# Kernel optimization log

Hardware: AMD Instinct MI355X
Metric: run time of the kernel (lower is better)

## Reference

```python
import jax, jax.numpy as jnp
import numpy as np

N = 8192
E = 262144
IN_F = 256
OUT_F = 64
H = 2
SLOPE = 0.2
NEG = -9e15


def _xavier(key, shape, gain):
    fan_in, fan_out = shape[-2], shape[-1]
    a = gain * np.sqrt(6.0 / (fan_in + fan_out))
    return jax.random.uniform(key, shape, jnp.float32, -a, a)


def setup_inputs() -> dict:
    key = jax.random.key(0)
    k_x, k_e, k_w, k_a1, k_a2 = jax.random.split(key, 5)
    gain = np.sqrt(2.0)
    return {
        "x": jax.random.normal(k_x, (N, IN_F), jnp.float32),
        "edge_index": jax.random.randint(k_e, (2, E), 0, N, jnp.int64),
        # per-head params (torch Linear stores weight [out,in]; we store [in,out])
        "W": _xavier(k_w, (H, IN_F, OUT_F), gain),
        "a1": _xavier(k_a1, (H, OUT_F), gain),
        "a2": _xavier(k_a2, (H, OUT_F), gain),
    }


def reference(x, edge_index, W, a1, a2):
    n = x.shape[0]
    # dense adjacency mask from COO edges (to_dense_adj: adj[src, dst] += 1; only adj>0 matters)
    adj = jnp.zeros((n, n), jnp.float32).at[edge_index[0], edge_index[1]].add(1.0)
    mask = adj > 0  # [N, N]

    xh = jnp.einsum('ni,hio->hno', x, W)          # [H, N, out]
    s1 = jnp.einsum('hno,ho->hn', xh, a1)          # a1(x): [H, N]
    s2 = jnp.einsum('hno,ho->hn', xh, a2)          # a2(x): [H, N]
    e = jnp.where(mask[None], s1[:, :, None] + s2[:, None, :], NEG)  # [H, N, N]
    e = jnp.where(e >= 0, e, SLOPE * e)            # leaky_relu
    att = jax.nn.softmax(e, axis=-1)               # [H, N, N]
    out = jnp.einsum('hnm,hmo->hno', att, xh)      # [H, N, out]
    # concat heads along feature dim (is_final_layer=False)
    return jnp.transpose(out, (1, 0, 2)).reshape(n, H * OUT_F)
```

## Files before the change

kernel.cpp:

```cpp
#include <hip/hip_runtime.h>

#define NN    8192
#define INF_  256
#define OUTF  64
#define NH    2
#define NE    262144
#define CAP   256
#define SLOPE 0.2f

typedef __attribute__((ext_vector_type(8))) short short8;
typedef __attribute__((ext_vector_type(4))) float f32x4;
typedef __attribute__((ext_vector_type(2))) long long ll2;

__device__ __forceinline__ unsigned short f2bf(float f) {
  unsigned int u = __float_as_uint(f);
  u += 0x7fffu + ((u >> 16) & 1u);
  return (unsigned short)(u >> 16);
}

__global__ __launch_bounds__(256) void prep_kernel(const float* __restrict__ W,
                                                   const unsigned int* __restrict__ ei,
                                                   unsigned short* __restrict__ Bt,
                                                   int* __restrict__ deg,
                                                   int* __restrict__ flag) {
  const int b = blockIdx.x, t = threadIdx.x;
  if (b < 128) {
    const int c = b, k = t;
    Bt[c * 256 + k] = f2bf(W[(c >> 6) * (INF_ * OUTF) + k * OUTF + (c & 63)]);
  } else if (b < 160) {
    deg[(b - 128) * 256 + t] = 0;
  } else {
    __shared__ int nz;
    if (t == 0) nz = 0;
    __syncthreads();
    if (ei[2u * t + 1u] != 0u) atomicAdd(&nz, 1);
    __syncthreads();
    if (t == 0) *flag = (nz == 0) ? 1 : 0;
  }
}

__global__ __launch_bounds__(256) void xh_mfma_kernel(const float* __restrict__ x,
                                                      const unsigned short* __restrict__ Bt,
                                                      const float* __restrict__ a1,
                                                      const float* __restrict__ a2,
                                                      float* __restrict__ xh,
                                                      float* __restrict__ s1,
                                                      float* __restrict__ s2) {
  const int t = threadIdx.x;
  const int l = t & 63, w = t >> 6;
  const int lo = l & 15, hi = l >> 4;
  const int n0 = blockIdx.x * 16;
  const int tcb = w * 2;
  __shared__ float p1s[4][16], p2s[4][16];

  const float* xp = x + (size_t)(n0 + lo) * INF_ + hi * 8;
  float4 fr[16];
#pragma unroll
  for (int ks = 0; ks < 8; ++ks) {
    fr[2 * ks]     = *(const float4*)(xp + ks * 32);
    fr[2 * ks + 1] = *(const float4*)(xp + ks * 32 + 4);
  }
  short8 afr[8];
#pragma unroll
  for (int ks = 0; ks < 8; ++ks) {
    short8 a;
    a[0] = (short)f2bf(fr[2 * ks].x);     a[1] = (short)f2bf(fr[2 * ks].y);
    a[2] = (short)f2bf(fr[2 * ks].z);     a[3] = (short)f2bf(fr[2 * ks].w);
    a[4] = (short)f2bf(fr[2 * ks + 1].x); a[5] = (short)f2bf(fr[2 * ks + 1].y);
    a[6] = (short)f2bf(fr[2 * ks + 1].z); a[7] = (short)f2bf(fr[2 * ks + 1].w);
    afr[ks] = a;
  }
  f32x4 acc[2] = {};
#pragma unroll
  for (int ks = 0; ks < 8; ++ks) {
#pragma unroll
    for (int q = 0; q < 2; ++q) {
      const short8 bf = *(const short8*)(Bt + (size_t)((tcb + q) * 16 + lo) * INF_ + ks * 32 + hi * 8);
      acc[q] = __builtin_amdgcn_mfma_f32_16x16x32_bf16(afr[ks], bf, acc[q], 0, 0, 0);
    }
  }
  float a1c[2], a2c[2];
#pragma unroll
  for (int q = 0; q < 2; ++q) {
    const int tc = tcb + q;
    const int h = tc >> 2;
    const int col = (tc * 16 + lo) & 63;
    a1c[q] = a1[h * OUTF + col];
    a2c[q] = a2[h * OUTF + col];
#pragma unroll
    for (int r = 0; r < 4; ++r)
      xh[((size_t)h * NN + n0 + hi * 4 + r) * OUTF + col] = acc[q][r];
  }
#pragma unroll
  for (int r = 0; r < 4; ++r) {
    float p1 = acc[0][r] * a1c[0] + acc[1][r] * a1c[1];
    float p2 = acc[0][r] * a2c[0] + acc[1][r] * a2c[1];
#pragma unroll
    for (int s = 1; s < 16; s <<= 1) {
      p1 += __shfl_xor(p1, s, 64);
      p2 += __shfl_xor(p2, s, 64);
    }
    if (lo == 0) {
      p1s[w][hi * 4 + r] = p1;
      p2s[w][hi * 4 + r] = p2;
    }
  }
  __syncthreads();
  if (t < 16) {
    s1[n0 + t]      = p1s[0][t] + p1s[1][t];
    s1[NN + n0 + t] = p1s[2][t] + p1s[3][t];
    s2[n0 + t]      = p2s[0][t] + p2s[1][t];
    s2[NN + n0 + t] = p2s[2][t] + p2s[3][t];
  }
}

__global__ __launch_bounds__(256) void edge_kernel(const int* __restrict__ ei,
                                                   const int* __restrict__ flag,
                                                   int* __restrict__ deg,
                                                   int* __restrict__ cols) {
  const int e0 = (blockIdx.x * 256 + threadIdx.x) * 2;
  if (e0 >= NE) return;
  int i0, j0, i1, j1;
  if (*flag) {
    const ll2 a = *(const ll2*)((const long long*)ei + e0);
    const ll2 b = *(const ll2*)((const long long*)ei + NE + e0);
    i0 = (int)a[0]; i1 = (int)a[1]; j0 = (int)b[0]; j1 = (int)b[1];
  } else {
    const int2 a = *(const int2*)(ei + e0);
    const int2 b = *(const int2*)(ei + NE + e0);
    i0 = a.x; i1 = a.y; j0 = b.x; j1 = b.y;
  }
  const int p0 = atomicAdd(&deg[i0], 1);
  if (p0 < CAP) cols[i0 * CAP + p0] = j0;
  const int p1 = atomicAdd(&deg[i1], 1);
  if (p1 < CAP) cols[i1 * CAP + p1] = j1;
}

__global__ __launch_bounds__(128) void agg_kernel(const float* __restrict__ xh,
                                                  const float* __restrict__ s1,
                                                  const float* __restrict__ s2,
                                                  const int* __restrict__ deg,
                                                  const int* __restrict__ cols,
                                                  float* __restrict__ out) {
  const int i = blockIdx.x;
  const int t = threadIdx.x;
  const int h = t >> 6, lane = t & 63;
  __shared__ unsigned int bm[NN / 32];
  __shared__ unsigned long long vmask;
  __shared__ int   cjs[CAP];
  __shared__ float wts[NH][CAP];
  int d = deg[i];
  if (d > CAP) d = CAP;
  bm[t] = 0u; bm[t + 128] = 0u;
  __syncthreads();

  const float* base = xh + (size_t)h * NN * OUTF;
  const int c4 = lane & 15, r = lane >> 4;

  if (d == 0) {
    f32x4 acc = {0.f, 0.f, 0.f, 0.f};
    for (int p = r; p < NN; p += 4)
      acc += *(const f32x4*)(base + (size_t)p * OUTF + 4 * c4);
#pragma unroll
    for (int c = 0; c < 4; ++c) {
      acc[c] += __shfl_xor(acc[c], 16, 64);
      acc[c] += __shfl_xor(acc[c], 32, 64);
    }
    if (lane < 16) {
      const float sc = 1.f / (float)NN;
      float4 o;
      o.x = acc[0] * sc; o.y = acc[1] * sc; o.z = acc[2] * sc; o.w = acc[3] * sc;
      *(float4*)(out + (size_t)i * (NH * OUTF) + h * OUTF + 4 * lane) = o;
    }
    return;
  }

  if (d <= 64) {
    int j = 0;
    const bool valid = lane < d;
    if (valid) j = cols[i * CAP + lane];
    if (h == 0) {
      bool dup = false;
      if (valid) {
        const unsigned int old = atomicOr(&bm[j >> 5], 1u << (j & 31));
        dup = (old >> (j & 31)) & 1u;
      }
      const unsigned long long bal = __ballot(valid && !dup);
      if (lane == 0) vmask = bal;
    }
    __syncthreads();
    const bool kp = (vmask >> lane) & 1ull;
    float sc = -1e30f;
    if (kp) {
      sc = s1[h * NN + i] + s2[h * NN + j];
      sc = (sc >= 0.f) ? sc : SLOPE * sc;
    }
    float m = sc;
#pragma unroll
    for (int s = 32; s > 0; s >>= 1) m = fmaxf(m, __shfl_xor(m, s, 64));
    const float wt = kp ? __expf(sc - m) : 0.f;
    float ds = wt;
#pragma unroll
    for (int s = 32; s > 0; s >>= 1) ds += __shfl_xor(ds, s, 64);
    const float inv = 1.f / ds;

    f32x4 acc = {0.f, 0.f, 0.f, 0.f};
#pragma unroll 2
    for (int p = 0; p < d; p += 4) {
      const int pr = p + r;
      float ww = __shfl(wt, pr, 64);
      int   jj = __shfl(j,  pr, 64);
      ww = (pr < d) ? ww : 0.f;
      jj = (ww > 0.f) ? jj : 0;
      const f32x4 v = *(const f32x4*)(base + (size_t)jj * OUTF + 4 * c4);
      acc += ww * v;
    }
#pragma unroll
    for (int c = 0; c < 4; ++c) {
      acc[c] += __shfl_xor(acc[c], 16, 64);
      acc[c] += __shfl_xor(acc[c], 32, 64);
    }
    if (lane < 16) {
      float4 o;
      o.x = acc[0] * inv; o.y = acc[1] * inv; o.z = acc[2] * inv; o.w = acc[3] * inv;
      *(float4*)(out + (size_t)i * (NH * OUTF) + h * OUTF + 4 * lane) = o;
    }
    return;
  }

  for (int p = t; p < d; p += 128) cjs[p] = cols[i * CAP + p];
  __syncthreads();
  if (h == 0) {
    for (int p = lane; p < d; p += 64) {
      const int j = cjs[p];
      const unsigned int old = atomicOr(&bm[j >> 5], 1u << (j & 31));
      if ((old >> (j & 31)) & 1u) cjs[p] = -1;
    }
  }
  __syncthreads();
  const float s1i = s1[h * NN + i];
  float m = -1e30f;
  for (int p = lane; p < d; p += 64) {
    const int j = cjs[p];
    float sc = -1e30f;
    if (j >= 0) {
      sc = s1i + s2[h * NN + j];
      sc = (sc >= 0.f) ? sc : SLOPE * sc;
    }
    wts[h][p] = sc;
    m = fmaxf(m, sc);
  }
#pragma unroll
  for (int s = 32; s > 0; s >>= 1) m = fmaxf(m, __shfl_xor(m, s, 64));
  float ds = 0.f;
  for (int p = lane; p < d; p += 64) {
    const float sc = wts[h][p];
    const float w2 = (sc > -1e29f) ? __expf(sc - m) : 0.f;
    wts[h][p] = w2;
    ds += w2;
  }
#pragma unroll
  for (int s = 32; s > 0; s >>= 1) ds += __shfl_xor(ds, s, 64);
  const float inv = 1.f / ds;
  float acc = 0.f;
  for (int p = 0; p < d; ++p) {
    const float w2 = wts[h][p];
    if (w2 > 0.f) acc += w2 * base[(size_t)cjs[p] * OUTF + lane];
  }
  out[(size_t)i * (NH * OUTF) + h * OUTF + lane] = acc * inv;
}

extern "C" void kernel_launch(void* const* d_in, const int* in_sizes, int n_in,
                              void* d_out, int out_size, void* d_ws, size_t ws_size,
                              hipStream_t stream) {
  const float* x  = (const float*)d_in[0];
  const int*   ei = (const int*)d_in[1];
  const float* W  = (const float*)d_in[2];
  const float* a1 = (const float*)d_in[3];
  const float* a2 = (const float*)d_in[4];
  float* out = (float*)d_out;

  char* ws = (char*)d_ws;
  float*          xh  = (float*)(ws);
  float*          s1  = (float*)(ws + (4u << 20));
  float*          s2  = (float*)(ws + (4u << 20) + (64u << 10));
  int*            deg = (int*)  (ws + (4u << 20) + (128u << 10));
  int*            cols= (int*)  (ws + (4u << 20) + (192u << 10));
  unsigned short* Bt  = (unsigned short*)(ws + (12u << 20) + (192u << 10));
  int*            flag= (int*)  (ws + (12u << 20) + (256u << 10));

  prep_kernel<<<161, 256, 0, stream>>>(W, (const unsigned int*)ei, Bt, deg, flag);
  xh_mfma_kernel<<<NN / 16, 256, 0, stream>>>(x, Bt, a1, a2, xh, s1, s2);
  edge_kernel<<<NE / 512, 256, 0, stream>>>(ei, flag, deg, cols);
  agg_kernel<<<NN, 128, 0, stream>>>(xh, s1, s2, deg, cols, out);
}
```

Measured before the change: 52.47 us.

## Map one wavefront per node-head task and pad degree counters to cut atomic contention

The aggregation kernel changes from one 128-thread block per node to a grid-stride loop that gives each wavefront one (node, head) task. Duplicate detection moves from an LDS bitmap with atomics and block syncs to a shuffle-based pairwise compare, and the large-degree path now recomputes scores instead of staging them in shared memory. Degree counters are padded to a 16-int stride so atomics on different nodes land on separate cache lines, and s1/s2 are stored interleaved per head as float2. The aim is to remove block-level syncs, the LDS bitmap clear, and atomic contention, at the cost of quadratic dedup work on high-degree nodes.

```diff
diff --git a/kernel.cpp b/kernel.cpp
--- a/kernel.cpp
+++ b/kernel.cpp
@@ -6,6 +6,7 @@
 #define NH    2
 #define NE    262144
 #define CAP   256
+#define DEGS  16
 #define SLOPE 0.2f
 
 typedef __attribute__((ext_vector_type(8))) short short8;
@@ -28,7 +29,9 @@
     const int c = b, k = t;
     Bt[c * 256 + k] = f2bf(W[(c >> 6) * (INF_ * OUTF) + k * OUTF + (c & 63)]);
   } else if (b < 160) {
-    deg[(b - 128) * 256 + t] = 0;
+    int4* dp = (int4*)(deg + (size_t)(b - 128) * 4096 + t * 16);
+    const int4 z = {0, 0, 0, 0};
+    dp[0] = z; dp[1] = z; dp[2] = z; dp[3] = z;
   } else {
     __shared__ int nz;
     if (t == 0) nz = 0;
@@ -44,8 +47,8 @@
                                                       const float* __restrict__ a1,
                                                       const float* __restrict__ a2,
                                                       float* __restrict__ xh,
-                                                      float* __restrict__ s1,
-                                                      float* __restrict__ s2) {
+                                                      float2* __restrict__ s1v,
+                                                      float2* __restrict__ s2v) {
   const int t = threadIdx.x;
   const int l = t & 63, w = t >> 6;
   const int lo = l & 15, hi = l >> 4;
@@ -107,10 +110,11 @@
   }
   __syncthreads();
   if (t < 16) {
-    s1[n0 + t]      = p1s[0][t] + p1s[1][t];
-    s1[NN + n0 + t] = p1s[2][t] + p1s[3][t];
-    s2[n0 + t]      = p2s[0][t] + p2s[1][t];
-    s2[NN + n0 + t] = p2s[2][t] + p2s[3][t];
+    float2 v1, v2;
+    v1.x = p1s[0][t] + p1s[1][t];  v1.y = p1s[2][t] + p1s[3][t];
+    v2.x = p2s[0][t] + p2s[1][t];  v2.y = p2s[2][t] + p2s[3][t];
+    s1v[n0 + t] = v1;
+    s2v[n0 + t] = v2;
   }
 }
 
@@ -130,90 +134,117 @@
     const int2 b = *(const int2*)(ei + NE + e0);
     i0 = a.x; i1 = a.y; j0 = b.x; j1 = b.y;
   }
-  const int p0 = atomicAdd(&deg[i0], 1);
+  const int p0 = atomicAdd(&deg[i0 * DEGS], 1);
   if (p0 < CAP) cols[i0 * CAP + p0] = j0;
-  const int p1 = atomicAdd(&deg[i1], 1);
+  const int p1 = atomicAdd(&deg[i1 * DEGS], 1);
   if (p1 < CAP) cols[i1 * CAP + p1] = j1;
 }
 
-__global__ __launch_bounds__(128) void agg_kernel(const float* __restrict__ xh,
-                                                  const float* __restrict__ s1,
-                                                  const float* __restrict__ s2,
+__global__ __launch_bounds__(256) void agg_kernel(const float* __restrict__ xh,
+                                                  const float2* __restrict__ s1v,
+                                                  const float2* __restrict__ s2v,
                                                   const int* __restrict__ deg,
                                                   const int* __restrict__ cols,
                                                   float* __restrict__ out) {
-  const int i = blockIdx.x;
   const int t = threadIdx.x;
-  const int h = t >> 6, lane = t & 63;
-  __shared__ unsigned int bm[NN / 32];
-  __shared__ unsigned long long vmask;
-  __shared__ int   cjs[CAP];
-  __shared__ float wts[NH][CAP];
-  int d = deg[i];
-  if (d > CAP) d = CAP;
-  bm[t] = 0u; bm[t + 128] = 0u;
-  __syncthreads();
-
-  const float* base = xh + (size_t)h * NN * OUTF;
+  const int w = t >> 6, lane = t & 63;
+  const int gw = blockIdx.x * 4 + w;
   const int c4 = lane & 15, r = lane >> 4;
 
-  if (d == 0) {
+  for (int task = gw; task < NN * NH; task += 8192) {
+    const int i = task >> 1, h = task & 1;
+    int d0 = deg[i * DEGS];
+    if (d0 > CAP) d0 = CAP;
+    const int d = __builtin_amdgcn_readfirstlane(d0);
+    const float* base = xh + (size_t)h * NN * OUTF;
     f32x4 acc = {0.f, 0.f, 0.f, 0.f};
-    for (int p = r; p < NN; p += 4)
-      acc += *(const f32x4*)(base + (size_t)p * OUTF + 4 * c4);
-#pragma unroll
-    for (int c = 0; c < 4; ++c) {
-      acc[c] += __shfl_xor(acc[c], 16, 64);
-      acc[c] += __shfl_xor(acc[c], 32, 64);
-    }
-    if (lane < 16) {
-      const float sc = 1.f / (float)NN;
-      float4 o;
-      o.x = acc[0] * sc; o.y = acc[1] * sc; o.z = acc[2] * sc; o.w = acc[3] * sc;
-      *(float4*)(out + (size_t)i * (NH * OUTF) + h * OUTF + 4 * lane) = o;
-    }
-    return;
-  }
-
-  if (d <= 64) {
-    int j = 0;
-    const bool valid = lane < d;
-    if (valid) j = cols[i * CAP + lane];
-    if (h == 0) {
+    float inv;
+
+    if (d == 0) {
+      for (int p = r; p < NN; p += 4)
+        acc += *(const f32x4*)(base + (size_t)p * OUTF + 4 * c4);
+      inv = 1.f / (float)NN;
+    } else if (d <= 64) {
+      const bool valid = lane < d;
+      int j = 0;
+      if (valid) j = cols[i * CAP + lane];
       bool dup = false;
-      if (valid) {
-        const unsigned int old = atomicOr(&bm[j >> 5], 1u << (j & 31));
-        dup = (old >> (j & 31)) & 1u;
-      }
-      const unsigned long long bal = __ballot(valid && !dup);
-      if (lane == 0) vmask = bal;
-    }
-    __syncthreads();
-    const bool kp = (vmask >> lane) & 1ull;
-    float sc = -1e30f;
-    if (kp) {
-      sc = s1[h * NN + i] + s2[h * NN + j];
-      sc = (sc >= 0.f) ? sc : SLOPE * sc;
-    }
-    float m = sc;
-#pragma unroll
-    for (int s = 32; s > 0; s >>= 1) m = fmaxf(m, __shfl_xor(m, s, 64));
-    const float wt = kp ? __expf(sc - m) : 0.f;
-    float ds = wt;
-#pragma unroll
-    for (int s = 32; s > 0; s >>= 1) ds += __shfl_xor(ds, s, 64);
-    const float inv = 1.f / ds;
-
-    f32x4 acc = {0.f, 0.f, 0.f, 0.f};
+      for (int q = 0; q < d; ++q) {
+        const int jq = __shfl(j, q, 64);
+        dup = dup || ((q < lane) && (jq == j));
+      }
+      const bool kp = valid && !dup;
+      float sc = -1e30f;
+      if (kp) {
+        const float2 s1i2 = s1v[i];
+        const float2 s2j2 = s2v[j];
+        sc = (h ? s1i2.y : s1i2.x) + (h ? s2j2.y : s2j2.x);
+        sc = (sc >= 0.f) ? sc : SLOPE * sc;
+      }
+      float m = sc;
+#pragma unroll
+      for (int s = 32; s > 0; s >>= 1) m = fmaxf(m, __shfl_xor(m, s, 64));
+      const float wt = kp ? __expf(sc - m) : 0.f;
+      float ds = wt;
+#pragma unroll
+      for (int s = 32; s > 0; s >>= 1) ds += __shfl_xor(ds, s, 64);
+      inv = 1.f / ds;
 #pragma unroll 2
-    for (int p = 0; p < d; p += 4) {
-      const int pr = p + r;
-      float ww = __shfl(wt, pr, 64);
-      int   jj = __shfl(j,  pr, 64);
-      ww = (pr < d) ? ww : 0.f;
-      jj = (ww > 0.f) ? jj : 0;
-      const f32x4 v = *(const f32x4*)(base + (size_t)jj * OUTF + 4 * c4);
-      acc += ww * v;
+      for (int p = 0; p < d; p += 4) {
+        const int pr = p + r;
+        float ww = __shfl(wt, pr, 64);
+        int   jj = __shfl(j,  pr, 64);
+        ww = (pr < d) ? ww : 0.f;
+        jj = (ww > 0.f) ? jj : 0;
+        acc += ww * *(const f32x4*)(base + (size_t)jj * OUTF + 4 * c4);
+      }
+    } else {
+      const float2 s1i2 = s1v[i];
+      const float s1i = h ? s1i2.y : s1i2.x;
+      float m = -1e30f;
+      for (int p = lane; p < d; p += 64) {
+        const int j = cols[i * CAP + p];
+        bool dup = false;
+        for (int q = 0; q < p; ++q)
+          if (cols[i * CAP + q] == j) { dup = true; break; }
+        if (!dup) {
+          const float2 s2j2 = s2v[j];
+          float sc = s1i + (h ? s2j2.y : s2j2.x);
+          sc = (sc >= 0.f) ? sc : SLOPE * sc;
+          m = fmaxf(m, sc);
+        }
+      }
+#pragma unroll
+      for (int s = 32; s > 0; s >>= 1) m = fmaxf(m, __shfl_xor(m, s, 64));
+      float ds = 0.f;
+      for (int p = lane; p < d; p += 64) {
+        const int j = cols[i * CAP + p];
+        bool dup = false;
+        for (int q = 0; q < p; ++q)
+          if (cols[i * CAP + q] == j) { dup = true; break; }
+        if (!dup) {
+          const float2 s2j2 = s2v[j];
+          float sc = s1i + (h ? s2j2.y : s2j2.x);
+          sc = (sc >= 0.f) ? sc : SLOPE * sc;
+          ds += __expf(sc - m);
+        }
+      }
+#pragma unroll
+      for (int s = 32; s > 0; s >>= 1) ds += __shfl_xor(ds, s, 64);
+      inv = 1.f / ds;
+      for (int p = 0; p < d; ++p) {
+        const int j = __shfl((lane == (p & 63)) ? cols[i * CAP + p] : 0, p & 63, 64);
+        bool dup = false;
+        for (int q = 0; q < p; ++q)
+          if (cols[i * CAP + q] == j) { dup = true; break; }
+        if (!dup) {
+          const float2 s2j2 = s2v[j];
+          float sc = s1i + (h ? s2j2.y : s2j2.x);
+          sc = (sc >= 0.f) ? sc : SLOPE * sc;
+          const float ww = __expf(sc - m);
+          acc += ww * *(const f32x4*)(base + (size_t)j * OUTF + 4 * c4);
+        }
+      }
     }
 #pragma unroll
     for (int c = 0; c < 4; ++c) {
@@ -225,49 +256,7 @@
       o.x = acc[0] * inv; o.y = acc[1] * inv; o.z = acc[2] * inv; o.w = acc[3] * inv;
       *(float4*)(out + (size_t)i * (NH * OUTF) + h * OUTF + 4 * lane) = o;
     }
-    return;
-  }
-
-  for (int p = t; p < d; p += 128) cjs[p] = cols[i * CAP + p];
-  __syncthreads();
-  if (h == 0) {
-    for (int p = lane; p < d; p += 64) {
-      const int j = cjs[p];
-      const unsigned int old = atomicOr(&bm[j >> 5], 1u << (j & 31));
-      if ((old >> (j & 31)) & 1u) cjs[p] = -1;
-    }
-  }
-  __syncthreads();
-  const float s1i = s1[h * NN + i];
-  float m = -1e30f;
-  for (int p = lane; p < d; p += 64) {
-    const int j = cjs[p];
-    float sc = -1e30f;
-    if (j >= 0) {
-      sc = s1i + s2[h * NN + j];
-      sc = (sc >= 0.f) ? sc : SLOPE * sc;
-    }
-    wts[h][p] = sc;
-    m = fmaxf(m, sc);
-  }
-#pragma unroll
-  for (int s = 32; s > 0; s >>= 1) m = fmaxf(m, __shfl_xor(m, s, 64));
-  float ds = 0.f;
-  for (int p = lane; p < d; p += 64) {
-    const float sc = wts[h][p];
-    const float w2 = (sc > -1e29f) ? __expf(sc - m) : 0.f;
-    wts[h][p] = w2;
-    ds += w2;
-  }
-#pragma unroll
-  for (int s = 32; s > 0; s >>= 1) ds += __shfl_xor(ds, s, 64);
-  const float inv = 1.f / ds;
-  float acc = 0.f;
-  for (int p = 0; p < d; ++p) {
-    const float w2 = wts[h][p];
-    if (w2 > 0.f) acc += w2 * base[(size_t)cjs[p] * OUTF + lane];
-  }
-  out[(size_t)i * (NH * OUTF) + h * OUTF + lane] = acc * inv;
+  }
 }
 
 extern "C" void kernel_launch(void* const* d_in, const int* in_sizes, int n_in,
@@ -282,15 +271,15 @@
 
   char* ws = (char*)d_ws;
   float*          xh  = (float*)(ws);
-  float*          s1  = (float*)(ws + (4u << 20));
-  float*          s2  = (float*)(ws + (4u << 20) + (64u << 10));
+  float2*         s1v = (float2*)(ws + (4u << 20));
+  float2*         s2v = (float2*)(ws + (4u << 20) + (64u << 10));
   int*            deg = (int*)  (ws + (4u << 20) + (128u << 10));
-  int*            cols= (int*)  (ws + (4u << 20) + (192u << 10));
-  unsigned short* Bt  = (unsigned short*)(ws + (12u << 20) + (192u << 10));
-  int*            flag= (int*)  (ws + (12u << 20) + (256u << 10));
+  int*            cols= (int*)  (ws + (5u << 20));
+  unsigned short* Bt  = (unsigned short*)(ws + (13u << 20));
+  int*            flag= (int*)  (ws + (13u << 20) + (64u << 10));
 
   prep_kernel<<<161, 256, 0, stream>>>(W, (const unsigned int*)ei, Bt, deg, flag);
-  xh_mfma_kernel<<<NN / 16, 256, 0, stream>>>(x, Bt, a1, a2, xh, s1, s2);
+  xh_mfma_kernel<<<NN / 16, 256, 0, stream>>>(x, Bt, a1, a2, xh, s1v, s2v);
   edge_kernel<<<NE / 512, 256, 0, stream>>>(ei, flag, deg, cols);
-  agg_kernel<<<NN, 128, 0, stream>>>(xh, s1, s2, deg, cols, out);
-}
+  agg_kernel<<<2048, 256, 0, stream>>>(xh, s1v, s2v, deg, cols, out);
+}
```

After: 58.04 us. 10.6% more time.
